# Optimization experiments

Hardware: AMD Instinct MI355X
Metric: run time of the kernel (lower is better)

Reference implementation:

```python
import jax, jax.numpy as jnp
import numpy as np

# Dense grid configuration (B, D, H, W) and channels C = nPlanes
B, D, H, W = 4, 64, 64, 64
C = 32
N_ACTIVE = 400000
N_SITES = B * D * H * W  # 1048576


def setup_inputs() -> dict:
    key = jax.random.key(0)
    k1, k2 = jax.random.split(key)
    features = jax.random.normal(k1, (N_ACTIVE, C), dtype=jnp.float32)
    flat_idx = jax.random.randint(k2, (N_ACTIVE,), 0, N_SITES, dtype=jnp.int64)
    return {"features": features, "flat_idx": flat_idx}


def reference(features, flat_idx):
    # Scatter sparse voxel features into the dense grid.
    # features: [N_active, C]; flat_idx: [N_active] linear index into B*D*H*W sites.
    dense = jnp.zeros((N_SITES, C), dtype=features.dtype)
    dense = dense.at[flat_idx].add(features)  # active sites are unique -> add == set
    # [B*D*H*W, C] -> [B, C, D, H, W] to match SCN's NCDHW dense layout
    return dense.reshape(B, D, H, W, C).transpose(0, 4, 1, 2, 3)
```

## Files before the change

kernel.cpp:

```cpp
#include <hip/hip_runtime.h>
#include <hip/hip_bf16.h>


#define DHW_LOG2 18
#define DHW (1 << DHW_LOG2)
#define C_CH 32
#define N_SITES_TOTAL (4 * DHW)

typedef float floatx4 __attribute__((ext_vector_type(4)));

__global__ __launch_bounds__(256) void init_head_kernel(int* __restrict__ head, int n)
{
    int t = blockIdx.x * blockDim.x + threadIdx.x;
    if (t < n) head[t] = -1;
}

__global__ __launch_bounds__(256) void build_chains_kernel(
    const int* __restrict__ flat_idx,
    int* __restrict__ head,
    int* __restrict__ next,
    int n_active)
{
    int i = blockIdx.x * blockDim.x + threadIdx.x;
    if (i >= n_active) return;
    int s = flat_idx[i];
    int prev = atomicExch(&head[s], i);
    next[i] = prev;
}

__global__ __launch_bounds__(256) void gather_kernel(
    const float* __restrict__ feats,
    const int* __restrict__ head,
    const int* __restrict__ next,
    float* __restrict__ out)
{
    int t = blockIdx.x * blockDim.x + threadIdx.x;
    int S = t >> 1;
    int h = t & 1;

    int b  = S >> DHW_LOG2;
    int sp = S & (DHW - 1);

    floatx4 a0 = (floatx4)0.f, a1 = (floatx4)0.f, a2 = (floatx4)0.f, a3 = (floatx4)0.f;

    int p = head[S];
    while (p != -1) {
        const floatx4* row = (const floatx4*)(feats + ((size_t)p * C_CH + h * 16));
        int pn = next[p];
        floatx4 f0 = row[0];
        floatx4 f1 = row[1];
        floatx4 f2 = row[2];
        floatx4 f3 = row[3];
        a0 += f0; a1 += f1; a2 += f2; a3 += f3;
        p = pn;
    }

    float* o = out + (((size_t)(b * C_CH + h * 16)) << DHW_LOG2) + sp;
    float acc[16] = {
        a0.x, a0.y, a0.z, a0.w,  a1.x, a1.y, a1.z, a1.w,
        a2.x, a2.y, a2.z, a2.w,  a3.x, a3.y, a3.z, a3.w };
    #pragma unroll
    for (int j = 0; j < 16; ++j)
        __builtin_nontemporal_store(acc[j], o + ((size_t)j << DHW_LOG2));
}

__global__ __launch_bounds__(256) void zero_kernel(float4* __restrict__ out, int n4)
{
    int t = blockIdx.x * blockDim.x + threadIdx.x;
    if (t < n4) out[t] = make_float4(0.f, 0.f, 0.f, 0.f);
}

__global__ __launch_bounds__(256) void scatter_atomic_kernel(
    const float* __restrict__ feats,
    const int* __restrict__ flat_idx,
    float* __restrict__ out,
    int n_active)
{
    int t = blockIdx.x * blockDim.x + threadIdx.x;
    int i = t >> 5, c = t & 31;
    if (i >= n_active) return;
    int s = flat_idx[i];
    atomicAdd(&out[(((size_t)(s >> DHW_LOG2) * C_CH + c) << DHW_LOG2) + (s & (DHW - 1))],
              feats[(size_t)i * C_CH + c]);
}

extern "C" void kernel_launch(void* const* d_in, const int* in_sizes, int n_in,
                              void* d_out, int out_size, void* d_ws, size_t ws_size,
                              hipStream_t stream) {
    const float* feats = (const float*)d_in[0];
    const int*   idx   = (const int*)d_in[1];
    float*       out   = (float*)d_out;
    int n_active = in_sizes[1];

    size_t head_bytes = (size_t)N_SITES_TOTAL * sizeof(int);
    size_t next_bytes = (size_t)n_active * sizeof(int);

    if (ws_size >= head_bytes + next_bytes) {
        int* head = (int*)d_ws;
        int* next = (int*)((char*)d_ws + head_bytes);

        init_head_kernel<<<(N_SITES_TOTAL + 255) / 256, 256, 0, stream>>>(head, N_SITES_TOTAL);
        build_chains_kernel<<<(n_active + 255) / 256, 256, 0, stream>>>(idx, head, next, n_active);
        gather_kernel<<<(2 * N_SITES_TOTAL) / 256, 256, 0, stream>>>(feats, head, next, out);
    } else {
        int n4 = out_size >> 2;
        zero_kernel<<<(n4 + 255) / 256, 256, 0, stream>>>((float4*)out, n4);
        int total = n_active * C_CH;
        scatter_atomic_kernel<<<(total + 255) / 256, 256, 0, stream>>>(feats, idx, out, n_active);
    }
}
```

Measured before the change: 203.6 us.

## Fuse init, chain build and gather into one cooperative grid-synced kernel

Replaces the three separate launches (head init, chain build, gather) with a single persistent cooperative kernel that grid-strides over each phase and separates them with grid-wide syncs. The head init also writes int2 pairs. This is meant to remove inter-kernel launch and drain gaps. In exchange it adds two grid barriers and limits the grid to the co-resident block count, which may reduce latency hiding in the memory-bound gather. It falls back to the original kernels if the cooperative launch fails.

```diff
diff --git a/kernel.cpp b/kernel.cpp
--- a/kernel.cpp
+++ b/kernel.cpp
@@ -1,5 +1,5 @@
 #include <hip/hip_runtime.h>
-#include <hip/hip_bf16.h>
+#include <hip/hip_cooperative_groups.h>
 
 
 #define DHW_LOG2 18
@@ -8,6 +8,66 @@
 #define N_SITES_TOTAL (4 * DHW)
 
 typedef float floatx4 __attribute__((ext_vector_type(4)));
+
+namespace cg = cooperative_groups;
+
+__global__ __launch_bounds__(256, 8) void fused_kernel(
+    const float* __restrict__ feats,
+    const int* __restrict__ flat_idx,
+    int* __restrict__ head,
+    int* __restrict__ next,
+    float* __restrict__ out,
+    int n_active)
+{
+    cg::grid_group grid = cg::this_grid();
+    const int tid0 = blockIdx.x * blockDim.x + threadIdx.x;
+    const int nthr = gridDim.x * blockDim.x;
+
+    int2* head2 = (int2*)head;
+    for (int i = tid0; i < N_SITES_TOTAL / 2; i += nthr)
+        head2[i] = make_int2(-1, -1);
+
+    grid.sync();
+
+    for (int i = tid0; i < n_active; i += nthr) {
+        int s = flat_idx[i];
+        int prev = atomicExch(&head[s], i);
+        next[i] = prev;
+    }
+
+    grid.sync();
+
+    for (int t = tid0; t < 2 * N_SITES_TOTAL; t += nthr) {
+        int S = t >> 1;
+        int h = t & 1;
+
+        int b  = S >> DHW_LOG2;
+        int sp = S & (DHW - 1);
+
+        floatx4 a0 = (floatx4)0.f, a1 = (floatx4)0.f, a2 = (floatx4)0.f, a3 = (floatx4)0.f;
+
+        int p = head[S];
+        while (p != -1) {
+            const floatx4* row = (const floatx4*)(feats + ((size_t)p * C_CH + h * 16));
+            int pn = next[p];
+            floatx4 f0 = row[0];
+            floatx4 f1 = row[1];
+            floatx4 f2 = row[2];
+            floatx4 f3 = row[3];
+            a0 += f0; a1 += f1; a2 += f2; a3 += f3;
+            p = pn;
+        }
+
+        float* o = out + (((size_t)(b * C_CH + h * 16)) << DHW_LOG2) + sp;
+        float acc[16] = {
+            a0.x, a0.y, a0.z, a0.w,  a1.x, a1.y, a1.z, a1.w,
+            a2.x, a2.y, a2.z, a2.w,  a3.x, a3.y, a3.z, a3.w };
+        #pragma unroll
+        for (int j = 0; j < 16; ++j)
+            __builtin_nontemporal_store(acc[j], o + ((size_t)j << DHW_LOG2));
+    }
+}
+
 
 __global__ __launch_bounds__(256) void init_head_kernel(int* __restrict__ head, int n)
 {
@@ -99,9 +159,25 @@
         int* head = (int*)d_ws;
         int* next = (int*)((char*)d_ws + head_bytes);
 
-        init_head_kernel<<<(N_SITES_TOTAL + 255) / 256, 256, 0, stream>>>(head, N_SITES_TOTAL);
-        build_chains_kernel<<<(n_active + 255) / 256, 256, 0, stream>>>(idx, head, next, n_active);
-        gather_kernel<<<(2 * N_SITES_TOTAL) / 256, 256, 0, stream>>>(feats, head, next, out);
+        int maxB = 0;
+        hipError_t qe = hipOccupancyMaxActiveBlocksPerMultiprocessor(
+            &maxB, fused_kernel, 256, 0);
+        int nblocks = 2048;
+        if (qe == hipSuccess && maxB > 0) {
+            int cap = maxB * 256;
+            if (cap < nblocks) nblocks = cap;
+        }
+
+        void* args[] = { (void*)&feats, (void*)&idx, (void*)&head,
+                         (void*)&next, (void*)&out, (void*)&n_active };
+        hipError_t le = hipLaunchCooperativeKernel(
+            fused_kernel, dim3(nblocks), dim3(256), args, 0, stream);
+
+        if (le != hipSuccess) {
+            init_head_kernel<<<(N_SITES_TOTAL + 255) / 256, 256, 0, stream>>>(head, N_SITES_TOTAL);
+            build_chains_kernel<<<(n_active + 255) / 256, 256, 0, stream>>>(idx, head, next, n_active);
+            gather_kernel<<<(2 * N_SITES_TOTAL) / 256, 256, 0, stream>>>(feats, head, next, out);
+        }
     } else {
         int n4 = out_size >> 2;
         zero_kernel<<<(n4 + 255) / 256, 256, 0, stream>>>((float4*)out, n4);
```

New measurement: 413.9 us. 2.03x slower.
